# Optimization experiments

Measured on AMD Instinct MI355X. Metric: run time of the kernel, lower is better.

The kernel has to match this reference:

```python
import jax, jax.numpy as jnp
import numpy as np

T, IN_DIM, H1, H2 = 64, 84, 128, 84
BATCH = 8192


def _glorot(key, shape, fan):
    bound = 1.0 / np.sqrt(fan)
    return jax.random.uniform(key, shape, jnp.float32, -bound, bound)


def setup_inputs() -> dict:
    key = jax.random.key(0)
    ks = jax.random.split(key, 13)
    x = jax.random.normal(ks[0], (BATCH, T, IN_DIM, 1), jnp.float32)
    # rnn1 layer 0: 84 -> 128
    w_ih_l0 = _glorot(ks[1], (H1, IN_DIM), H1)
    w_hh_l0 = _glorot(ks[2], (H1, H1), H1)
    b_ih_l0 = _glorot(ks[3], (H1,), H1)
    b_hh_l0 = _glorot(ks[4], (H1,), H1)
    # rnn1 layer 1: 128 -> 128
    w_ih_l1 = _glorot(ks[5], (H1, H1), H1)
    w_hh_l1 = _glorot(ks[6], (H1, H1), H1)
    b_ih_l1 = _glorot(ks[7], (H1,), H1)
    b_hh_l1 = _glorot(ks[8], (H1,), H1)
    # rnn2: 128 -> 84
    w_ih_l2 = _glorot(ks[9], (H2, H1), H2)
    w_hh_l2 = _glorot(ks[10], (H2, H2), H2)
    b_ih_l2 = _glorot(ks[11], (H2,), H2)
    b_hh_l2 = _glorot(ks[12], (H2,), H2)
    return {
        "x": x,
        "w_ih_l0": w_ih_l0, "w_hh_l0": w_hh_l0, "b_ih_l0": b_ih_l0, "b_hh_l0": b_hh_l0,
        "w_ih_l1": w_ih_l1, "w_hh_l1": w_hh_l1, "b_ih_l1": b_ih_l1, "b_hh_l1": b_hh_l1,
        "w_ih_l2": w_ih_l2, "w_hh_l2": w_hh_l2, "b_ih_l2": b_ih_l2, "b_hh_l2": b_hh_l2,
    }


def _elman_layer(x, w_ih, w_hh, b_ih, b_hh):
    # x: (B, T, I) -> (B, T, H); h_t = tanh(x_t W_ih^T + b_ih + h_{t-1} W_hh^T + b_hh)
    # Precompute the input projection for all timesteps as one big GEMM.
    xp = jnp.einsum('bti,hi->bth', x, w_ih) + (b_ih + b_hh)  # (B, T, H)
    h0 = jnp.zeros((x.shape[0], w_hh.shape[0]), x.dtype)

    def step(h, xp_t):
        h = jnp.tanh(xp_t + h @ w_hh.T)
        return h, h

    _, ys = jax.lax.scan(step, h0, jnp.swapaxes(xp, 0, 1))  # (T, B, H)
    return jnp.swapaxes(ys, 0, 1)


def reference(x,
              w_ih_l0, w_hh_l0, b_ih_l0, b_hh_l0,
              w_ih_l1, w_hh_l1, b_ih_l1, b_hh_l1,
              w_ih_l2, w_hh_l2, b_ih_l2, b_hh_l2):
    x_ = jnp.squeeze(x, -1)                                   # (B, 64, 84)
    h = _elman_layer(x_, w_ih_l0, w_hh_l0, b_ih_l0, b_hh_l0)  # (B, 64, 128)
    h = _elman_layer(h, w_ih_l1, w_hh_l1, b_ih_l1, b_hh_l1)   # (B, 64, 128)
    h = _elman_layer(h, w_ih_l2, w_hh_l2, b_ih_l2, b_hh_l2)   # (B, 64, 84)
    return h[..., None]                                       # (B, 64, 84, 1)
```

## Files before the change

### kernel.cpp

```cpp
#include <hip/hip_runtime.h>


typedef __bf16 bf16x8 __attribute__((ext_vector_type(8)));
typedef float  f32x4  __attribute__((ext_vector_type(4)));
typedef unsigned short u16;
typedef unsigned int   u32;
typedef u16 u16x8 __attribute__((ext_vector_type(8)));

#define MFMA16(a, b, c) __builtin_amdgcn_mfma_f32_16x16x32_bf16((a), (b), (c), 0, 0, 0)

__device__ __forceinline__ float bf2f(u16 v) {
    return __builtin_bit_cast(float, (u32)v << 16);
}
__device__ __forceinline__ u16 f2bf(float f) {
    u32 u = __builtin_bit_cast(u32, f);
    u = u + 0x7fffu + ((u >> 16) & 1u);
    return (u16)(u >> 16);
}
__device__ __forceinline__ float tanh_fast(float x) {
    float xc = fminf(fmaxf(x, -12.f), 12.f);
    float e  = __expf(2.f * xc);
    return (e - 1.f) * __builtin_amdgcn_rcpf(e + 1.f);
}
__device__ __forceinline__ f32x4 splat4(float v) {
    f32x4 r; r[0] = v; r[1] = v; r[2] = v; r[3] = v; return r;
}
__device__ __forceinline__ bf16x8 ld_lds8(const u16* p) {
    return __builtin_bit_cast(bf16x8, *(const u16x8*)p);
}
__device__ __forceinline__ void store_hl(u16* ph, u16* pl, float v) {
    u16 hi = f2bf(v);
    *ph = hi;
    *pl = f2bf(v - bf2f(hi));
}

struct fragp { bf16x8 h, l; };

__device__ __forceinline__ fragp load_wfrag_hl(const float* W, int Hr, int Kr,
                                               int n, int kbase) {
    u16x8 uh = {0,0,0,0,0,0,0,0}, ul = {0,0,0,0,0,0,0,0};
    if (n < Hr) {
#pragma unroll
        for (int j = 0; j < 8; j++) {
            int k = kbase + j;
            if (k < Kr) {
                float w = W[n * Kr + k];
                u16 hi = f2bf(w);
                uh[j] = hi;
                ul[j] = f2bf(w - bf2f(hi));
            }
        }
    }
    fragp r;
    r.h = __builtin_bit_cast(bf16x8, uh);
    r.l = __builtin_bit_cast(bf16x8, ul);
    return r;
}

__device__ __forceinline__ f32x4 mm3(bf16x8 ah, bf16x8 al, const fragp& b, f32x4 c) {
    c = MFMA16(ah, b.h, c);
    c = MFMA16(ah, b.l, c);
    c = MFMA16(al, b.h, c);
    return c;
}

__global__ __launch_bounds__(512, 2)
void rnn_fused(const float* __restrict__ x,
               const float* __restrict__ wih0, const float* __restrict__ whh0,
               const float* __restrict__ bih0, const float* __restrict__ bhh0,
               const float* __restrict__ wih1, const float* __restrict__ whh1,
               const float* __restrict__ bih1, const float* __restrict__ bhh1,
               const float* __restrict__ wih2, const float* __restrict__ whh2,
               const float* __restrict__ bih2, const float* __restrict__ bhh2,
               float* __restrict__ out)
{
    __shared__ __align__(16) u16 h0h[2][32][136], h0l[2][32][136];
    __shared__ __align__(16) u16 h1h[2][32][136], h1l[2][32][136];
    __shared__ __align__(16) u16 h2h[2][32][104], h2l[2][32][104];
    __shared__ __align__(16) u16 xbh[2][32][96],  xbl[2][32][96];
    __shared__ __align__(16) float xpT[2][128][32];

    const int tid  = threadIdx.x;
    const int wv   = tid >> 6;
    const int lane = tid & 63;
    const int ln   = lane & 15;
    const int q    = lane >> 4;
    const int aw   = wv & 3;
    const bool isA = (wv < 4);
    const int xsw  = (ln & 7) << 2;
    const int b0   = blockIdx.x * 32;
    const float* xg = x + (long)b0 * 5376;

    const int col0 = aw * 32 + ln;
    const int col1 = aw * 32 + 16 + ln;

    { u16* z = &h0h[1][0][0]; for (int i = tid; i < 32 * 136; i += 512) z[i] = 0; }
    { u16* z = &h0l[1][0][0]; for (int i = tid; i < 32 * 136; i += 512) z[i] = 0; }
    { u16* z = &h1h[0][0][0]; for (int i = tid; i < 32 * 136; i += 512) z[i] = 0; }
    { u16* z = &h1l[0][0][0]; for (int i = tid; i < 32 * 136; i += 512) z[i] = 0; }
    { u16* z = &h2h[1][0][0]; for (int i = tid; i < 32 * 104; i += 512) z[i] = 0; }
    { u16* z = &h2l[1][0][0]; for (int i = tid; i < 32 * 104; i += 512) z[i] = 0; }
    for (int i = tid; i < 32 * 12 * 2; i += 512) {
        int par = i / (32 * 12), rem = i - par * 32 * 12;
        int row = rem / 12, col = 84 + rem - row * 12;
        xbh[par][row][col] = 0; xbl[par][row][col] = 0;
    }
    for (int i = tid; i < 32 * 84; i += 512) {
        int row = i / 84, col = i - row * 84;
        float v = xg[(long)row * 5376 + col];
        u16 hi = f2bf(v);
        xbh[0][row][col] = hi;
        xbl[0][row][col] = f2bf(v - bf2f(hi));
    }

    __syncthreads();

    if (isA) {
        fragp fhh0[2][4], fih2[2][4], fhh2[2][3];
#pragma unroll
        for (int c = 0; c < 4; c++) {
            fhh0[0][c] = load_wfrag_hl(whh0, 128, 128, col0, c * 32 + q * 8);
            fhh0[1][c] = load_wfrag_hl(whh0, 128, 128, col1, c * 32 + q * 8);
            fih2[0][c] = load_wfrag_hl(wih2,  84, 128, col0, c * 32 + q * 8);
            fih2[1][c] = load_wfrag_hl(wih2,  84, 128, col1, c * 32 + q * 8);
        }
#pragma unroll
        for (int c = 0; c < 3; c++) {
            fhh2[0][c] = load_wfrag_hl(whh2, 84, 84, col0, c * 32 + q * 8);
            fhh2[1][c] = load_wfrag_hl(whh2, 84, 84, col1, c * 32 + q * 8);
        }
        const float bias2c[2] = { (col0 < 84) ? bih2[col0] + bhh2[col0] : 0.f,
                                  (col1 < 84) ? bih2[col1] + bhh2[col1] : 0.f };

        f32x4 acc[2][2];
        float xs[6];

        for (int rr = 0; rr < 67; ++rr) {
            const int P = rr & 1, PN = P ^ 1;

            if (rr <= 62) {
#pragma unroll
                for (int j = 0; j < 6; j++) {
                    int i = tid + j * 512;
                    if (i < 2688) {
                        int row = i / 84, cc = i - row * 84;
                        xs[j] = xg[(long)row * 5376 + (rr + 1) * 84 + cc];
                    }
                }
            }

            if (rr >= 1 && rr <= 64) {
#pragma unroll
                for (int n2 = 0; n2 < 2; n2++) {
                    const int colx = aw * 32 + n2 * 16 + ln;
                    acc[n2][0] = *(const f32x4*)&xpT[P][colx][(4 * q) ^ xsw];
                    acc[n2][1] = *(const f32x4*)&xpT[P][colx][(16 + 4 * q) ^ xsw];
                }
                __builtin_amdgcn_s_setprio(1);
#pragma unroll
                for (int c = 0; c < 4; c++) {
                    const int off = c * 32 + q * 8;
                    bf16x8 a0h = ld_lds8(&h0h[P][ln][off]),      a0l = ld_lds8(&h0l[P][ln][off]);
                    bf16x8 a1h = ld_lds8(&h0h[P][16 + ln][off]), a1l = ld_lds8(&h0l[P][16 + ln][off]);
                    acc[0][0] = mm3(a0h, a0l, fhh0[0][c], acc[0][0]);
                    acc[1][0] = mm3(a0h, a0l, fhh0[1][c], acc[1][0]);
                    acc[0][1] = mm3(a1h, a1l, fhh0[0][c], acc[0][1]);
                    acc[1][1] = mm3(a1h, a1l, fhh0[1][c], acc[1][1]);
                }
                __builtin_amdgcn_s_setprio(0);
#pragma unroll
                for (int r = 0; r < 4; r++) {
                    const int row = q * 4 + r;
                    store_hl(&h0h[PN][row     ][col0], &h0l[PN][row     ][col0], tanh_fast(acc[0][0][r]));
                    store_hl(&h0h[PN][row     ][col1], &h0l[PN][row     ][col1], tanh_fast(acc[1][0][r]));
                    store_hl(&h0h[PN][16 + row][col0], &h0l[PN][16 + row][col0], tanh_fast(acc[0][1][r]));
                    store_hl(&h0h[PN][16 + row][col1], &h0l[PN][16 + row][col1], tanh_fast(acc[1][1][r]));
                }
            }

            if (aw != 3 && rr >= 3) {
                const int t2 = rr - 3;
                acc[0][0] = splat4(bias2c[0]); acc[0][1] = splat4(bias2c[0]);
                acc[1][0] = splat4(bias2c[1]); acc[1][1] = splat4(bias2c[1]);
                __builtin_amdgcn_s_setprio(1);
#pragma unroll
                for (int c = 0; c < 4; c++) {
                    const int off = c * 32 + q * 8;
                    bf16x8 a0h = ld_lds8(&h1h[P][ln][off]),      a0l = ld_lds8(&h1l[P][ln][off]);
                    bf16x8 a1h = ld_lds8(&h1h[P][16 + ln][off]), a1l = ld_lds8(&h1l[P][16 + ln][off]);
                    acc[0][0] = mm3(a0h, a0l, fih2[0][c], acc[0][0]);
                    acc[1][0] = mm3(a0h, a0l, fih2[1][c], acc[1][0]);
                    acc[0][1] = mm3(a1h, a1l, fih2[0][c], acc[0][1]);
                    acc[1][1] = mm3(a1h, a1l, fih2[1][c], acc[1][1]);
                }
#pragma unroll
                for (int c = 0; c < 3; c++) {
                    const int off = c * 32 + q * 8;
                    bf16x8 a0h = ld_lds8(&h2h[P][ln][off]),      a0l = ld_lds8(&h2l[P][ln][off]);
                    bf16x8 a1h = ld_lds8(&h2h[P][16 + ln][off]), a1l = ld_lds8(&h2l[P][16 + ln][off]);
                    acc[0][0] = mm3(a0h, a0l, fhh2[0][c], acc[0][0]);
                    acc[1][0] = mm3(a0h, a0l, fhh2[1][c], acc[1][0]);
                    acc[0][1] = mm3(a1h, a1l, fhh2[0][c], acc[0][1]);
                    acc[1][1] = mm3(a1h, a1l, fhh2[1][c], acc[1][1]);
                }
                __builtin_amdgcn_s_setprio(0);
#pragma unroll
                for (int r = 0; r < 4; r++) {
                    const int row = q * 4 + r;
                    float v00 = tanh_fast(acc[0][0][r]);
                    float v10 = tanh_fast(acc[0][1][r]);
                    float v01 = tanh_fast(acc[1][0][r]);
                    float v11 = tanh_fast(acc[1][1][r]);
                    store_hl(&h2h[PN][row     ][col0], &h2l[PN][row     ][col0], v00);
                    store_hl(&h2h[PN][16 + row][col0], &h2l[PN][16 + row][col0], v10);
                    store_hl(&h2h[PN][row     ][col1], &h2l[PN][row     ][col1], v01);
                    store_hl(&h2h[PN][16 + row][col1], &h2l[PN][16 + row][col1], v11);
                    float* o0 = out + (long)(b0 + row)      * 5376 + t2 * 84;
                    float* o1 = out + (long)(b0 + 16 + row) * 5376 + t2 * 84;
                    if (col0 < 84) { o0[col0] = v00; o1[col0] = v10; }
                    if (col1 < 84) { o0[col1] = v01; o1[col1] = v11; }
                }
            }

            if (rr <= 62) {
#pragma unroll
                for (int j = 0; j < 6; j++) {
                    int i = tid + j * 512;
                    if (i < 2688) {
                        int row = i / 84, cc = i - row * 84;
                        u16 hi = f2bf(xs[j]);
                        xbh[PN][row][cc] = hi;
                        xbl[PN][row][cc] = f2bf(xs[j] - bf2f(hi));
                    }
                }
            }
            __syncthreads();
        }
    } else {
        fragp fih0[2][3], fih1[2][4], fhh1[2][4];
#pragma unroll
        for (int c = 0; c < 3; c++) {
            fih0[0][c] = load_wfrag_hl(wih0, 128, 84, col0, c * 32 + q * 8);
            fih0[1][c] = load_wfrag_hl(wih0, 128, 84, col1, c * 32 + q * 8);
        }
#pragma unroll
        for (int c = 0; c < 4; c++) {
            fih1[0][c] = load_wfrag_hl(wih1, 128, 128, col0, c * 32 + q * 8);
            fih1[1][c] = load_wfrag_hl(wih1, 128, 128, col1, c * 32 + q * 8);
            fhh1[0][c] = load_wfrag_hl(whh1, 128, 128, col0, c * 32 + q * 8);
            fhh1[1][c] = load_wfrag_hl(whh1, 128, 128, col1, c * 32 + q * 8);
        }
        const float bias0c[2] = { bih0[col0] + bhh0[col0], bih0[col1] + bhh0[col1] };
        const float bias1c[2] = { bih1[col0] + bhh1[col0], bih1[col1] + bhh1[col1] };

        f32x4 acc[2][2];
        float xs[6];

        for (int rr = 0; rr < 67; ++rr) {
            const int P = rr & 1, PN = P ^ 1;

            if (rr <= 62) {
#pragma unroll
                for (int j = 0; j < 6; j++) {
                    int i = tid + j * 512;
                    if (i < 2688) {
                        int row = i / 84, cc = i - row * 84;
                        xs[j] = xg[(long)row * 5376 + (rr + 1) * 84 + cc];
                    }
                }
            }

            if (rr >= 2 && rr <= 65) {
                acc[0][0] = splat4(bias1c[0]); acc[0][1] = splat4(bias1c[0]);
                acc[1][0] = splat4(bias1c[1]); acc[1][1] = splat4(bias1c[1]);
                __builtin_amdgcn_s_setprio(1);
#pragma unroll
                for (int c = 0; c < 4; c++) {
                    const int off = c * 32 + q * 8;
                    bf16x8 a0h = ld_lds8(&h0h[P][ln][off]),      a0l = ld_lds8(&h0l[P][ln][off]);
                    bf16x8 a1h = ld_lds8(&h0h[P][16 + ln][off]), a1l = ld_lds8(&h0l[P][16 + ln][off]);
                    acc[0][0] = mm3(a0h, a0l, fih1[0][c], acc[0][0]);
                    acc[1][0] = mm3(a0h, a0l, fih1[1][c], acc[1][0]);
                    acc[0][1] = mm3(a1h, a1l, fih1[0][c], acc[0][1]);
                    acc[1][1] = mm3(a1h, a1l, fih1[1][c], acc[1][1]);
                }
#pragma unroll
                for (int c = 0; c < 4; c++) {
                    const int off = c * 32 + q * 8;
                    bf16x8 a0h = ld_lds8(&h1h[P][ln][off]),      a0l = ld_lds8(&h1l[P][ln][off]);
                    bf16x8 a1h = ld_lds8(&h1h[P][16 + ln][off]), a1l = ld_lds8(&h1l[P][16 + ln][off]);
                    acc[0][0] = mm3(a0h, a0l, fhh1[0][c], acc[0][0]);
                    acc[1][0] = mm3(a0h, a0l, fhh1[1][c], acc[1][0]);
                    acc[0][1] = mm3(a1h, a1l, fhh1[0][c], acc[0][1]);
                    acc[1][1] = mm3(a1h, a1l, fhh1[1][c], acc[1][1]);
                }
                __builtin_amdgcn_s_setprio(0);
#pragma unroll
                for (int r = 0; r < 4; r++) {
                    const int row = q * 4 + r;
                    store_hl(&h1h[PN][row     ][col0], &h1l[PN][row     ][col0], tanh_fast(acc[0][0][r]));
                    store_hl(&h1h[PN][row     ][col1], &h1l[PN][row     ][col1], tanh_fast(acc[1][0][r]));
                    store_hl(&h1h[PN][16 + row][col0], &h1l[PN][16 + row][col0], tanh_fast(acc[0][1][r]));
                    store_hl(&h1h[PN][16 + row][col1], &h1l[PN][16 + row][col1], tanh_fast(acc[1][1][r]));
                }
            }

            if (rr <= 63) {
                acc[0][0] = splat4(bias0c[0]); acc[0][1] = splat4(bias0c[0]);
                acc[1][0] = splat4(bias0c[1]); acc[1][1] = splat4(bias0c[1]);
                __builtin_amdgcn_s_setprio(1);
#pragma unroll
                for (int c = 0; c < 3; c++) {
                    const int off = c * 32 + q * 8;
                    bf16x8 a0h = ld_lds8(&xbh[P][ln][off]),      a0l = ld_lds8(&xbl[P][ln][off]);
                    bf16x8 a1h = ld_lds8(&xbh[P][16 + ln][off]), a1l = ld_lds8(&xbl[P][16 + ln][off]);
                    acc[0][0] = mm3(a0h, a0l, fih0[0][c], acc[0][0]);
                    acc[1][0] = mm3(a0h, a0l, fih0[1][c], acc[1][0]);
                    acc[0][1] = mm3(a1h, a1l, fih0[0][c], acc[0][1]);
                    acc[1][1] = mm3(a1h, a1l, fih0[1][c], acc[1][1]);
                }
                __builtin_amdgcn_s_setprio(0);
#pragma unroll
                for (int n2 = 0; n2 < 2; n2++) {
                    const int colx = aw * 32 + n2 * 16 + ln;
                    *(f32x4*)&xpT[PN][colx][(4 * q) ^ xsw]      = acc[n2][0];
                    *(f32x4*)&xpT[PN][colx][(16 + 4 * q) ^ xsw] = acc[n2][1];
                }
            }

            if (rr <= 62) {
#pragma unroll
                for (int j = 0; j < 6; j++) {
                    int i = tid + j * 512;
                    if (i < 2688) {
                        int row = i / 84, cc = i - row * 84;
                        u16 hi = f2bf(xs[j]);
                        xbh[PN][row][cc] = hi;
                        xbl[PN][row][cc] = f2bf(xs[j] - bf2f(hi));
                    }
                }
            }
            __syncthreads();
        }
    }
}

extern "C" void kernel_launch(void* const* d_in, const int* in_sizes, int n_in,
                              void* d_out, int out_size, void* d_ws, size_t ws_size,
                              hipStream_t stream) {
    (void)in_sizes; (void)n_in; (void)out_size; (void)d_ws; (void)ws_size;
    const float* x    = (const float*)d_in[0];
    const float* wih0 = (const float*)d_in[1];
    const float* whh0 = (const float*)d_in[2];
    const float* bih0 = (const float*)d_in[3];
    const float* bhh0 = (const float*)d_in[4];
    const float* wih1 = (const float*)d_in[5];
    const float* whh1 = (const float*)d_in[6];
    const float* bih1 = (const float*)d_in[7];
    const float* bhh1 = (const float*)d_in[8];
    const float* wih2 = (const float*)d_in[9];
    const float* whh2 = (const float*)d_in[10];
    const float* bih2 = (const float*)d_in[11];
    const float* bhh2 = (const float*)d_in[12];
    float* out = (float*)d_out;

    rnn_fused<<<dim3(8192 / 32), dim3(512), 0, stream>>>(
        x, wih0, whh0, bih0, bhh0, wih1, whh1, bih1, bhh1,
        wih2, whh2, bih2, bhh2, out);
}
```

Before: 586.4 us.

## Switch recurrent MFMAs to 32x32x16 with transposed operands and swizzled LDS

Replaces the four 16x16x32 MFMA tiles per wave with a single 32x32x16 MFMA tile, computing W*h^T so each lane holds four consecutive hidden columns for one batch row. LDS hidden-state buffers move to an unpadded XOR-swizzled 128-wide layout. Stores become vectorized 4-element writes, including float4 global output stores. Biases are staged in LDS instead of registers. The aim is fewer MFMA issues and fewer LDS/global scalar stores, in exchange for more weight fragment registers and a different bank-conflict pattern.

After: 558.5 us. 4.8% less time.

```diff
diff --git a/kernel.cpp b/kernel.cpp
--- a/kernel.cpp
+++ b/kernel.cpp
@@ -3,11 +3,13 @@
 
 typedef __bf16 bf16x8 __attribute__((ext_vector_type(8)));
 typedef float  f32x4  __attribute__((ext_vector_type(4)));
+typedef float  f32x16 __attribute__((ext_vector_type(16)));
 typedef unsigned short u16;
 typedef unsigned int   u32;
 typedef u16 u16x8 __attribute__((ext_vector_type(8)));
-
-#define MFMA16(a, b, c) __builtin_amdgcn_mfma_f32_16x16x32_bf16((a), (b), (c), 0, 0, 0)
+typedef u16 u16x4 __attribute__((ext_vector_type(4)));
+
+#define MFMA32(a, b, c) __builtin_amdgcn_mfma_f32_32x32x16_bf16((a), (b), (c), 0, 0, 0)
 
 __device__ __forceinline__ float bf2f(u16 v) {
     return __builtin_bit_cast(float, (u32)v << 16);
@@ -22,16 +24,25 @@
     float e  = __expf(2.f * xc);
     return (e - 1.f) * __builtin_amdgcn_rcpf(e + 1.f);
 }
-__device__ __forceinline__ f32x4 splat4(float v) {
-    f32x4 r; r[0] = v; r[1] = v; r[2] = v; r[3] = v; return r;
-}
 __device__ __forceinline__ bf16x8 ld_lds8(const u16* p) {
     return __builtin_bit_cast(bf16x8, *(const u16x8*)p);
 }
-__device__ __forceinline__ void store_hl(u16* ph, u16* pl, float v) {
-    u16 hi = f2bf(v);
-    *ph = hi;
-    *pl = f2bf(v - bf2f(hi));
+__device__ __forceinline__ int aswz(int row, int off) {
+    return row * 128 + (off ^ ((row & 7) << 3));
+}
+__device__ __forceinline__ int xswz(int m, int n) {
+    return m * 128 + (n ^ ((m & 7) << 2));
+}
+__device__ __forceinline__ void store4_hl(u16* ph, u16* pl, f32x4 v) {
+    u16x4 hi, lo;
+#pragma unroll
+    for (int j = 0; j < 4; j++) {
+        u16 h = f2bf(v[j]);
+        hi[j] = h;
+        lo[j] = f2bf(v[j] - bf2f(h));
+    }
+    *(u16x4*)ph = hi;
+    *(u16x4*)pl = lo;
 }
 
 struct fragp { bf16x8 h, l; };
@@ -57,10 +68,10 @@
     return r;
 }
 
-__device__ __forceinline__ f32x4 mm3(bf16x8 ah, bf16x8 al, const fragp& b, f32x4 c) {
-    c = MFMA16(ah, b.h, c);
-    c = MFMA16(ah, b.l, c);
-    c = MFMA16(al, b.h, c);
+__device__ __forceinline__ f32x16 mm3t(const fragp& w, bf16x8 ah, bf16x8 al, f32x16 c) {
+    c = MFMA32(w.h, ah, c);
+    c = MFMA32(w.l, ah, c);
+    c = MFMA32(w.h, al, c);
     return c;
 }
 
@@ -74,32 +85,32 @@
                const float* __restrict__ bih2, const float* __restrict__ bhh2,
                float* __restrict__ out)
 {
-    __shared__ __align__(16) u16 h0h[2][32][136], h0l[2][32][136];
-    __shared__ __align__(16) u16 h1h[2][32][136], h1l[2][32][136];
-    __shared__ __align__(16) u16 h2h[2][32][104], h2l[2][32][104];
-    __shared__ __align__(16) u16 xbh[2][32][96],  xbl[2][32][96];
-    __shared__ __align__(16) float xpT[2][128][32];
+    __shared__ __align__(16) u16 h0h[2][4096], h0l[2][4096];
+    __shared__ __align__(16) u16 h1h[2][4096], h1l[2][4096];
+    __shared__ __align__(16) u16 h2h[2][4096], h2l[2][4096];
+    __shared__ __align__(16) u16 xbh[2][32][96], xbl[2][32][96];
+    __shared__ __align__(16) float xpF[2][4096];
+    __shared__ float biasF[3][128];
 
     const int tid  = threadIdx.x;
     const int wv   = tid >> 6;
     const int lane = tid & 63;
-    const int ln   = lane & 15;
-    const int q    = lane >> 4;
+    const int mrow = lane & 31;
+    const int q2   = lane >> 5;
+    const int kq   = q2 * 8;
+    const int q4   = q2 * 4;
     const int aw   = wv & 3;
     const bool isA = (wv < 4);
-    const int xsw  = (ln & 7) << 2;
+    const int nb   = aw * 32;
     const int b0   = blockIdx.x * 32;
     const float* xg = x + (long)b0 * 5376;
 
-    const int col0 = aw * 32 + ln;
-    const int col1 = aw * 32 + 16 + ln;
-
-    { u16* z = &h0h[1][0][0]; for (int i = tid; i < 32 * 136; i += 512) z[i] = 0; }
-    { u16* z = &h0l[1][0][0]; for (int i = tid; i < 32 * 136; i += 512) z[i] = 0; }
-    { u16* z = &h1h[0][0][0]; for (int i = tid; i < 32 * 136; i += 512) z[i] = 0; }
-    { u16* z = &h1l[0][0][0]; for (int i = tid; i < 32 * 136; i += 512) z[i] = 0; }
-    { u16* z = &h2h[1][0][0]; for (int i = tid; i < 32 * 104; i += 512) z[i] = 0; }
-    { u16* z = &h2l[1][0][0]; for (int i = tid; i < 32 * 104; i += 512) z[i] = 0; }
+    { u16* z = &h0h[1][0]; for (int i = tid; i < 4096; i += 512) z[i] = 0; }
+    { u16* z = &h0l[1][0]; for (int i = tid; i < 4096; i += 512) z[i] = 0; }
+    { u16* z = &h1h[0][0]; for (int i = tid; i < 4096; i += 512) z[i] = 0; }
+    { u16* z = &h1l[0][0]; for (int i = tid; i < 4096; i += 512) z[i] = 0; }
+    { u16* z = &h2h[1][0]; for (int i = tid; i < 4096; i += 512) z[i] = 0; }
+    { u16* z = &h2l[1][0]; for (int i = tid; i < 4096; i += 512) z[i] = 0; }
     for (int i = tid; i < 32 * 12 * 2; i += 512) {
         int par = i / (32 * 12), rem = i - par * 32 * 12;
         int row = rem / 12, col = 84 + rem - row * 12;
@@ -112,29 +123,29 @@
         xbh[0][row][col] = hi;
         xbl[0][row][col] = f2bf(v - bf2f(hi));
     }
+    for (int i = tid; i < 384; i += 512) {
+        int l = i >> 7, n = i & 127;
+        float v = 0.f;
+        if (l == 0)      v = bih0[n] + bhh0[n];
+        else if (l == 1) v = bih1[n] + bhh1[n];
+        else if (n < 84) v = bih2[n] + bhh2[n];
+        biasF[l][n] = v;
+    }
 
     __syncthreads();
 
     if (isA) {
-        fragp fhh0[2][4], fih2[2][4], fhh2[2][3];
-#pragma unroll
-        for (int c = 0; c < 4; c++) {
-            fhh0[0][c] = load_wfrag_hl(whh0, 128, 128, col0, c * 32 + q * 8);
-            fhh0[1][c] = load_wfrag_hl(whh0, 128, 128, col1, c * 32 + q * 8);
-            fih2[0][c] = load_wfrag_hl(wih2,  84, 128, col0, c * 32 + q * 8);
-            fih2[1][c] = load_wfrag_hl(wih2,  84, 128, col1, c * 32 + q * 8);
-        }
-#pragma unroll
-        for (int c = 0; c < 3; c++) {
-            fhh2[0][c] = load_wfrag_hl(whh2, 84, 84, col0, c * 32 + q * 8);
-            fhh2[1][c] = load_wfrag_hl(whh2, 84, 84, col1, c * 32 + q * 8);
-        }
-        const float bias2c[2] = { (col0 < 84) ? bih2[col0] + bhh2[col0] : 0.f,
-                                  (col1 < 84) ? bih2[col1] + bhh2[col1] : 0.f };
-
-        f32x4 acc[2][2];
+        fragp fhh0[8], fih2[8], fhh2[6];
+#pragma unroll
+        for (int c = 0; c < 8; c++) {
+            fhh0[c] = load_wfrag_hl(whh0, 128, 128, nb + mrow, c * 16 + kq);
+            fih2[c] = load_wfrag_hl(wih2,  84, 128, nb + mrow, c * 16 + kq);
+        }
+#pragma unroll
+        for (int c = 0; c < 6; c++)
+            fhh2[c] = load_wfrag_hl(whh2, 84, 84, nb + mrow, c * 16 + kq);
+
         float xs[6];
-
         for (int rr = 0; rr < 67; ++rr) {
             const int P = rr & 1, PN = P ^ 1;
 
@@ -150,75 +161,62 @@
             }
 
             if (rr >= 1 && rr <= 64) {
-#pragma unroll
-                for (int n2 = 0; n2 < 2; n2++) {
-                    const int colx = aw * 32 + n2 * 16 + ln;
-                    acc[n2][0] = *(const f32x4*)&xpT[P][colx][(4 * q) ^ xsw];
-                    acc[n2][1] = *(const f32x4*)&xpT[P][colx][(16 + 4 * q) ^ xsw];
+                f32x16 acc;
+#pragma unroll
+                for (int g = 0; g < 4; g++) {
+                    f32x4 v = *(const f32x4*)&xpF[P][xswz(mrow, nb + g * 8 + q4)];
+                    acc[4*g+0] = v[0]; acc[4*g+1] = v[1];
+                    acc[4*g+2] = v[2]; acc[4*g+3] = v[3];
                 }
                 __builtin_amdgcn_s_setprio(1);
 #pragma unroll
-                for (int c = 0; c < 4; c++) {
-                    const int off = c * 32 + q * 8;
-                    bf16x8 a0h = ld_lds8(&h0h[P][ln][off]),      a0l = ld_lds8(&h0l[P][ln][off]);
-                    bf16x8 a1h = ld_lds8(&h0h[P][16 + ln][off]), a1l = ld_lds8(&h0l[P][16 + ln][off]);
-                    acc[0][0] = mm3(a0h, a0l, fhh0[0][c], acc[0][0]);
-                    acc[1][0] = mm3(a0h, a0l, fhh0[1][c], acc[1][0]);
-                    acc[0][1] = mm3(a1h, a1l, fhh0[0][c], acc[0][1]);
-                    acc[1][1] = mm3(a1h, a1l, fhh0[1][c], acc[1][1]);
+                for (int c = 0; c < 8; c++) {
+                    const int idx = aswz(mrow, c * 16 + kq);
+                    acc = mm3t(fhh0[c], ld_lds8(&h0h[P][idx]), ld_lds8(&h0l[P][idx]), acc);
                 }
                 __builtin_amdgcn_s_setprio(0);
 #pragma unroll
-                for (int r = 0; r < 4; r++) {
-                    const int row = q * 4 + r;
-                    store_hl(&h0h[PN][row     ][col0], &h0l[PN][row     ][col0], tanh_fast(acc[0][0][r]));
-                    store_hl(&h0h[PN][row     ][col1], &h0l[PN][row     ][col1], tanh_fast(acc[1][0][r]));
-                    store_hl(&h0h[PN][16 + row][col0], &h0l[PN][16 + row][col0], tanh_fast(acc[0][1][r]));
-                    store_hl(&h0h[PN][16 + row][col1], &h0l[PN][16 + row][col1], tanh_fast(acc[1][1][r]));
+                for (int g = 0; g < 4; g++) {
+                    const int col = nb + g * 8 + q4;
+                    f32x4 v;
+                    v[0] = tanh_fast(acc[4*g+0]); v[1] = tanh_fast(acc[4*g+1]);
+                    v[2] = tanh_fast(acc[4*g+2]); v[3] = tanh_fast(acc[4*g+3]);
+                    const int idx = mrow * 128 + (col ^ ((mrow & 7) << 3));
+                    store4_hl(&h0h[PN][idx], &h0l[PN][idx], v);
                 }
             }
 
             if (aw != 3 && rr >= 3) {
                 const int t2 = rr - 3;
-                acc[0][0] = splat4(bias2c[0]); acc[0][1] = splat4(bias2c[0]);
-                acc[1][0] = splat4(bias2c[1]); acc[1][1] = splat4(bias2c[1]);
+                f32x16 acc;
+#pragma unroll
+                for (int g = 0; g < 4; g++) {
+                    f32x4 v = *(const f32x4*)&biasF[2][nb + g * 8 + q4];
+                    acc[4*g+0] = v[0]; acc[4*g+1] = v[1];
+                    acc[4*g+2] = v[2]; acc[4*g+3] = v[3];
+                }
                 __builtin_amdgcn_s_setprio(1);
 #pragma unroll
-                for (int c = 0; c < 4; c++) {
-                    const int off = c * 32 + q * 8;
-                    bf16x8 a0h = ld_lds8(&h1h[P][ln][off]),      a0l = ld_lds8(&h1l[P][ln][off]);
-                    bf16x8 a1h = ld_lds8(&h1h[P][16 + ln][off]), a1l = ld_lds8(&h1l[P][16 + ln][off]);
-                    acc[0][0] = mm3(a0h, a0l, fih2[0][c], acc[0][0]);
-                    acc[1][0] = mm3(a0h, a0l, fih2[1][c], acc[1][0]);
-                    acc[0][1] = mm3(a1h, a1l, fih2[0][c], acc[0][1]);
-                    acc[1][1] = mm3(a1h, a1l, fih2[1][c], acc[1][1]);
-                }
-#pragma unroll
-                for (int c = 0; c < 3; c++) {
-                    const int off = c * 32 + q * 8;
-                    bf16x8 a0h = ld_lds8(&h2h[P][ln][off]),      a0l = ld_lds8(&h2l[P][ln][off]);
-                    bf16x8 a1h = ld_lds8(&h2h[P][16 + ln][off]), a1l = ld_lds8(&h2l[P][16 + ln][off]);
-                    acc[0][0] = mm3(a0h, a0l, fhh2[0][c], acc[0][0]);
-                    acc[1][0] = mm3(a0h, a0l, fhh2[1][c], acc[1][0]);
-                    acc[0][1] = mm3(a1h, a1l, fhh2[0][c], acc[0][1]);
-                    acc[1][1] = mm3(a1h, a1l, fhh2[1][c], acc[1][1]);
+                for (int c = 0; c < 8; c++) {
+                    const int idx = aswz(mrow, c * 16 + kq);
+                    acc = mm3t(fih2[c], ld_lds8(&h1h[P][idx]), ld_lds8(&h1l[P][idx]), acc);
+                }
+#pragma unroll
+                for (int c = 0; c < 6; c++) {
+                    const int idx = aswz(mrow, c * 16 + kq);
+                    acc = mm3t(fhh2[c], ld_lds8(&h2h[P][idx]), ld_lds8(&h2l[P][idx]), acc);
                 }
                 __builtin_amdgcn_s_setprio(0);
 #pragma unroll
-                for (int r = 0; r < 4; r++) {
-                    const int row = q * 4 + r;
-                    float v00 = tanh_fast(acc[0][0][r]);
-                    float v10 = tanh_fast(acc[0][1][r]);
-                    float v01 = tanh_fast(acc[1][0][r]);
-                    float v11 = tanh_fast(acc[1][1][r]);
-                    store_hl(&h2h[PN][row     ][col0], &h2l[PN][row     ][col0], v00);
-                    store_hl(&h2h[PN][16 + row][col0], &h2l[PN][16 + row][col0], v10);
-                    store_hl(&h2h[PN][row     ][col1], &h2l[PN][row     ][col1], v01);
-                    store_hl(&h2h[PN][16 + row][col1], &h2l[PN][16 + row][col1], v11);
-                    float* o0 = out + (long)(b0 + row)      * 5376 + t2 * 84;
-                    float* o1 = out + (long)(b0 + 16 + row) * 5376 + t2 * 84;
-                    if (col0 < 84) { o0[col0] = v00; o1[col0] = v10; }
-                    if (col1 < 84) { o0[col1] = v01; o1[col1] = v11; }
+                for (int g = 0; g < 4; g++) {
+                    const int col = nb + g * 8 + q4;
+                    f32x4 v;
+                    v[0] = tanh_fast(acc[4*g+0]); v[1] = tanh_fast(acc[4*g+1]);
+                    v[2] = tanh_fast(acc[4*g+2]); v[3] = tanh_fast(acc[4*g+3]);
+                    const int idx = mrow * 128 + (col ^ ((mrow & 7) << 3));
+                    store4_hl(&h2h[PN][idx], &h2l[PN][idx], v);
+                    if (col < 84)
+                        *(f32x4*)(out + (long)(b0 + mrow) * 5376 + t2 * 84 + col) = v;
                 }
             }
 
@@ -237,25 +235,17 @@
             __syncthreads();
         }
     } else {
-        fragp fih0[2][3], fih1[2][4], fhh1[2][4];
-#pragma unroll
-        for (int c = 0; c < 3; c++) {
-            fih0[0][c] = load_wfrag_hl(wih0, 128, 84, col0, c * 32 + q * 8);
-            fih0[1][c] = load_wfrag_hl(wih0, 128, 84, col1, c * 32 + q * 8);
-        }
-#pragma unroll
-        for (int c = 0; c < 4; c++) {
-            fih1[0][c] = load_wfrag_hl(wih1, 128, 128, col0, c * 32 + q * 8);
-            fih1[1][c] = load_wfrag_hl(wih1, 128, 128, col1, c * 32 + q * 8);
-            fhh1[0][c] = load_wfrag_hl(whh1, 128, 128, col0, c * 32 + q * 8);
-            fhh1[1][c] = load_wfrag_hl(whh1, 128, 128, col1, c * 32 + q * 8);
-        }
-        const float bias0c[2] = { bih0[col0] + bhh0[col0], bih0[col1] + bhh0[col1] };
-        const float bias1c[2] = { bih1[col0] + bhh1[col0], bih1[col1] + bhh1[col1] };
-
-        f32x4 acc[2][2];
+        fragp fih0[6], fih1[8], fhh1[8];
+#pragma unroll
+        for (int c = 0; c < 6; c++)
+            fih0[c] = load_wfrag_hl(wih0, 128, 84, nb + mrow, c * 16 + kq);
+#pragma unroll
+        for (int c = 0; c < 8; c++) {
+            fih1[c] = load_wfrag_hl(wih1, 128, 128, nb + mrow, c * 16 + kq);
+            fhh1[c] = load_wfrag_hl(whh1, 128, 128, nb + mrow, c * 16 + kq);
+        }
+
         float xs[6];
-
         for (int rr = 0; rr < 67; ++rr) {
             const int P = rr & 1, PN = P ^ 1;
 
@@ -271,60 +261,60 @@
             }
 
             if (rr >= 2 && rr <= 65) {
-                acc[0][0] = splat4(bias1c[0]); acc[0][1] = splat4(bias1c[0]);
-                acc[1][0] = splat4(bias1c[1]); acc[1][1] = splat4(bias1c[1]);
+                f32x16 acc;
+#pragma unroll
+                for (int g = 0; g < 4; g++) {
+                    f32x4 v = *(const f32x4*)&biasF[1][nb + g * 8 + q4];
+                    acc[4*g+0] = v[0]; acc[4*g+1] = v[1];
+                    acc[4*g+2] = v[2]; acc[4*g+3] = v[3];
+                }
                 __builtin_amdgcn_s_setprio(1);
 #pragma unroll
-                for (int c = 0; c < 4; c++) {
-                    const int off = c * 32 + q * 8;
-                    bf16x8 a0h = ld_lds8(&h0h[P][ln][off]),      a0l = ld_lds8(&h0l[P][ln][off]);
-                    bf16x8 a1h = ld_lds8(&h0h[P][16 + ln][off]), a1l = ld_lds8(&h0l[P][16 + ln][off]);
-                    acc[0][0] = mm3(a0h, a0l, fih1[0][c], acc[0][0]);
-                    acc[1][0] = mm3(a0h, a0l, fih1[1][c], acc[1][0]);
-                    acc[0][1] = mm3(a1h, a1l, fih1[0][c], acc[0][1]);
-                    acc[1][1] = mm3(a1h, a1l, fih1[1][c], acc[1][1]);
-                }
-#pragma unroll
-                for (int c = 0; c < 4; c++) {
-                    const int off = c * 32 + q * 8;
-                    bf16x8 a0h = ld_lds8(&h1h[P][ln][off]),      a0l = ld_lds8(&h1l[P][ln][off]);
-                    bf16x8 a1h = ld_lds8(&h1h[P][16 + ln][off]), a1l = ld_lds8(&h1l[P][16 + ln][off]);
-                    acc[0][0] = mm3(a0h, a0l, fhh1[0][c], acc[0][0]);
-                    acc[1][0] = mm3(a0h, a0l, fhh1[1][c], acc[1][0]);
-                    acc[0][1] = mm3(a1h, a1l, fhh1[0][c], acc[0][1]);
-                    acc[1][1] = mm3(a1h, a1l, fhh1[1][c], acc[1][1]);
+                for (int c = 0; c < 8; c++) {
+                    const int idx = aswz(mrow, c * 16 + kq);
+                    acc = mm3t(fih1[c], ld_lds8(&h0h[P][idx]), ld_lds8(&h0l[P][idx]), acc);
+                }
+#pragma unroll
+                for (int c = 0; c < 8; c++) {
+                    const int idx = aswz(mrow, c * 16 + kq);
+                    acc = mm3t(fhh1[c], ld_lds8(&h1h[P][idx]), ld_lds8(&h1l[P][idx]), acc);
                 }
                 __builtin_amdgcn_s_setprio(0);
 #pragma unroll
-                for (int r = 0; r < 4; r++) {
-                    const int row = q * 4 + r;
-                    store_hl(&h1h[PN][row     ][col0], &h1l[PN][row     ][col0], tanh_fast(acc[0][0][r]));
-                    store_hl(&h1h[PN][row     ][col1], &h1l[PN][row     ][col1], tanh_fast(acc[1][0][r]));
-                    store_hl(&h1h[PN][16 + row][col0], &h1l[PN][16 + row][col0], tanh_fast(acc[0][1][r]));
-                    store_hl(&h1h[PN][16 + row][col1], &h1l[PN][16 + row][col1], tanh_fast(acc[1][1][r]));
+                for (int g = 0; g < 4; g++) {
+                    const int col = nb + g * 8 + q4;
+                    f32x4 v;
+                    v[0] = tanh_fast(acc[4*g+0]); v[1] = tanh_fast(acc[4*g+1]);
+                    v[2] = tanh_fast(acc[4*g+2]); v[3] = tanh_fast(acc[4*g+3]);
+                    const int idx = mrow * 128 + (col ^ ((mrow & 7) << 3));
+                    store4_hl(&h1h[PN][idx], &h1l[PN][idx], v);
                 }
             }
 
             if (rr <= 63) {
-                acc[0][0] = splat4(bias0c[0]); acc[0][1] = splat4(bias0c[0]);
-                acc[1][0] = splat4(bias0c[1]); acc[1][1] = splat4(bias0c[1]);
+                f32x16 acc;
+#pragma unroll
+                for (int g = 0; g < 4; g++) {
+                    f32x4 v = *(const f32x4*)&biasF[0][nb + g * 8 + q4];
+                    acc[4*g+0] = v[0]; acc[4*g+1] = v[1];
+                    acc[4*g+2] = v[2]; acc[4*g+3] = v[3];
+                }
                 __builtin_amdgcn_s_setprio(1);
 #pragma unroll
-                for (int c = 0; c < 3; c++) {
-                    const int off = c * 32 + q * 8;
-                    bf16x8 a0h = ld_lds8(&xbh[P][ln][off]),      a0l = ld_lds8(&xbl[P][ln][off]);
-                    bf16x8 a1h = ld_lds8(&xbh[P][16 + ln][off]), a1l = ld_lds8(&xbl[P][16 + ln][off]);
-                    acc[0][0] = mm3(a0h, a0l, fih0[0][c], acc[0][0]);
-                    acc[1][0] = mm3(a0h, a0l, fih0[1][c], acc[1][0]);
-                    acc[0][1] = mm3(a1h, a1l, fih0[0][c], acc[0][1]);
-                    acc[1][1] = mm3(a1h, a1l, fih0[1][c], acc[1][1]);
+                for (int c = 0; c < 6; c++) {
+                    const int off = c * 16 + kq;
+                    bf16x8 ah = ld_lds8(&xbh[P][mrow][off]);
+                    bf16x8 al = ld_lds8(&xbl[P][mrow][off]);
+                    acc = mm3t(fih0[c], ah, al, acc);
                 }
                 __builtin_amdgcn_s_setprio(0);
 #pragma unroll
-                for (int n2 = 0; n2 < 2; n2++) {
-                    const int colx = aw * 32 + n2 * 16 + ln;
-                    *(f32x4*)&xpT[PN][colx][(4 * q) ^ xsw]      = acc[n2][0];
-                    *(f32x4*)&xpT[PN][colx][(16 + 4 * q) ^ xsw] = acc[n2][1];
+                for (int g = 0; g < 4; g++) {
+                    const int n = nb + g * 8 + q4;
+                    f32x4 v;
+                    v[0] = acc[4*g+0]; v[1] = acc[4*g+1];
+                    v[2] = acc[4*g+2]; v[3] = acc[4*g+3];
+                    *(f32x4*)&xpF[PN][xswz(mrow, n)] = v;
                 }
             }
 
```
